# Performance work log

Hardware: AMD Instinct MI355X
Metric: run time of the kernel (lower is better)

The kernel has to match this reference:

```python
import jax, jax.numpy as jnp
import numpy as np
from jax import lax

CHANNEL = 64
HIDDEN = 128

def _conv(x, w, b):
    # x: [B, Cin, H, W], w: [Cout, Cin, 3, 3] -> [B, Cout, H, W], SAME padding
    y = lax.conv_general_dilated(x, w, window_strides=(1, 1), padding='SAME',
                                 dimension_numbers=('NCHW', 'OIHW', 'NCHW'))
    return y + b[None, :, None, None]

def setup_inputs() -> dict:
    key = jax.random.key(0)
    ks = jax.random.split(key, 5)
    T, B, C, H, W = 12, 2, CHANNEL, 128, 128
    x = jax.random.normal(ks[0], (T, B, C, H, W), dtype=jnp.float32)
    fan_g = (C + HIDDEN) * 9
    W_gates = jax.random.normal(ks[1], (4 * HIDDEN, C + HIDDEN, 3, 3), dtype=jnp.float32) / np.sqrt(fan_g)
    b_gates = jnp.zeros((4 * HIDDEN,), dtype=jnp.float32)
    W_out = jax.random.normal(ks[2], (C, HIDDEN, 3, 3), dtype=jnp.float32) / np.sqrt(HIDDEN * 9)
    b_out = jnp.zeros((C,), dtype=jnp.float32)
    return {'x': x, 'W_gates': W_gates, 'b_gates': b_gates, 'W_out': W_out, 'b_out': b_out}

def _convlstm_forward(x, W_gates, b_gates, W_out, b_out):
    T, B, C, H, W = x.shape
    h0 = jnp.zeros((B, HIDDEN, H, W), dtype=x.dtype)
    c0 = jnp.zeros((B, HIDDEN, H, W), dtype=x.dtype)

    def step(carry, xt):
        h, c = carry
        gates = _conv(jnp.concatenate([xt, h], axis=1), W_gates, b_gates)
        i_g, f_g, o_g, g_g = jnp.split(gates, 4, axis=1)
        c = jax.nn.sigmoid(f_g) * c + jax.nn.sigmoid(i_g) * jnp.tanh(g_g)
        h = jax.nn.sigmoid(o_g) * jnp.tanh(c)
        return (h, c), h

    _, hs = lax.scan(step, (h0, c0), x)          # hs: [T, B, HIDDEN, H, W]
    out = _conv(hs.reshape(T * B, HIDDEN, H, W), W_out, b_out)
    return out.reshape(T, B, C, H, W)

def reference(x, W_gates, b_gates, W_out, b_out):
    return _convlstm_forward(x, W_gates, b_gates, W_out, b_out)
```

## Files before the change

kernel.cpp:

```cpp
#include <hip/hip_runtime.h>

typedef _Float16 f16;
typedef __attribute__((ext_vector_type(8))) _Float16 f16x8;
typedef __attribute__((ext_vector_type(4))) float f32x4;
typedef __attribute__((ext_vector_type(16))) float f32x16;

#define SLICE_H 4326400


__device__ __forceinline__ void gld_lds16(void* lds, const void* g) {
  __builtin_amdgcn_global_load_lds(
      (const __attribute__((address_space(1))) void*)g,
      (__attribute__((address_space(3))) void*)lds, 16, 0, 0);
}

__device__ __forceinline__ float sigf(float v) { return 1.0f / (1.0f + __expf(-v)); }
__device__ __forceinline__ float tanh_fast(float v) { return 2.0f / (1.0f + __expf(-2.0f * v)) - 1.0f; }


__global__ __launch_bounds__(256) void kwt(const float* __restrict__ wsrc,
                                           f16* __restrict__ th, int R) {
  int idx = blockIdx.x * 256 + threadIdx.x;
  if (idx >= 9 * R) return;
  int tap = idx / R, r = idx - tap * R;
  th[idx] = (f16)wsrc[(size_t)r * 9 + tap];
}

__global__ __launch_bounds__(256) void kwtg(const float* __restrict__ wsrc,
                                            f16* __restrict__ th) {
  int idx = blockIdx.x * 256 + threadIdx.x;
  const int R = 512 * 192;
  if (idx >= 9 * R) return;
  int tap = idx / R, rr = idx - tap * R;
  int co = rr / 192, ci = rr - co * 192;
  int gate = co >> 7, hch = co & 127;
  int N = ((hch >> 6) << 8) + (((hch >> 5) & 1) << 7) + (gate << 5) + (hch & 31);
  th[(size_t)tap * R + (size_t)N * 192 + ci] = (f16)wsrc[(size_t)rr * 9 + tap];
}


__global__ __launch_bounds__(256) void kxform(const float* __restrict__ xt,
                                              f16* __restrict__ xp) {
  int pid = blockIdx.x * 256 + threadIdx.x;
  int b = pid >> 14, y = (pid >> 7) & 127, x = pid & 127;
  const float* src = xt + (size_t)b * 64 * 16384 + (size_t)y * 128 + x;
  size_t doff = ((size_t)((b * 130 + y + 1) * 130 + (x + 1))) * 64;
#pragma unroll
  for (int cc = 0; cc < 8; ++cc) {
    f16x8 vh;
#pragma unroll
    for (int j = 0; j < 8; ++j) vh[j] = (f16)src[(size_t)(cc * 8 + j) * 16384];
    *(f16x8*)(xp + doff + cc * 8) = vh;
  }
}


#define SMEM_G (25344 + 49152)

__global__ __launch_bounds__(256, 2) void kgates(
    const f16* __restrict__ xp, const f16* __restrict__ hp,
    const f16* __restrict__ wg, const float* __restrict__ bg,
    float* __restrict__ cbuf, f16* __restrict__ hslot) {
  extern __shared__ char smem[];
  f16* Ap = (f16*)smem;
  f16* Br = (f16*)(smem + 25344);
  const int tid = threadIdx.x;
  const int lane = tid & 63;
  const int w = tid >> 6;
  const int l31 = lane & 31;
  const int h5 = lane >> 5;
  const int wm = w >> 1, wn = w & 1;
  const int y = blockIdx.x;
  const int b = blockIdx.y;
  const int z = blockIdx.z;
  const int n0 = z * 256;
  const int chunk = (lane & 3) ^ ((lane >> 3) & 3);
  const int slotB0 = (h5 ^ ((l31 >> 1) & 3) ^ ((l31 >> 4) & 1)) << 3;

  f32x16 acc[2][4] = {};

  const f16* wgthr = wg + (size_t)(n0 + (lane >> 2)) * 192 +
                     (chunk ^ (w & 1)) * 8 + w * 3072;

  auto stageA = [&](int cig) {
    const f16* S; int CS, cigl;
    if (cig < 2) { S = xp; CS = 64;  cigl = cig; }
    else         { S = hp; CS = 128; cigl = cig - 2; }
    for (int i = w; i < 27; i += 4) {
      int dy = i / 9, sub = i - dy * 9;
      int xp0 = sub * 16;
      const f16* src = S +
          ((size_t)((b * 130 + y + dy) * 130 + xp0 + (lane >> 2))) * CS +
          cigl * 32 + (chunk ^ (sub & 1)) * 8;
      f16* dst = Ap + (dy * 132 + xp0) * 32;
      if (sub == 8) { if (lane < 16) gld_lds16(dst, src); }
      else gld_lds16(dst, src);
    }
  };
  auto stageB = [&](int j) {
    int cig = j / 9, tap = j - cig * 9;
    f16* dst = Br + (j % 3) * 8192 + w * 512;
    const f16* src = wgthr + (size_t)tap * (512 * 192) + cig * 32;
#pragma unroll
    for (int ii = 0; ii < 4; ++ii)
      gld_lds16(dst + ii * 2048, src + ii * 12288);
  };

  stageA(0);
  stageB(0);
  stageB(1);
  asm volatile("s_waitcnt vmcnt(4)" ::: "memory");
  __builtin_amdgcn_s_barrier();

  for (int j = 0; j < 54; ++j) {
    const int cig = j / 9, tap = j - cig * 9;
    const int dy = tap / 3, dx = tap - dy * 3;

    if (j + 2 < 54) stageB(j + 2);

    const f16* Bc = Br + (j % 3) * 8192;
    const int rr = l31 + dx;
    const int slotA0 = (h5 ^ ((rr >> 1) & 3) ^ ((rr >> 4) & 1)) << 3;
    const f16* arow = Ap + dy * (132 * 32) + (wm * 64 + rr) * 32;
    const f16* brow = Bc + (wn * 128 + l31) * 32;
    f16x8 af[2][2], bfr[4][2];
#pragma unroll
    for (int mt = 0; mt < 2; ++mt) {
      af[mt][0] = *(const f16x8*)(arow + mt * 1024 + slotA0);
      af[mt][1] = *(const f16x8*)(arow + mt * 1024 + (slotA0 ^ 16));
    }
#pragma unroll
    for (int nt = 0; nt < 4; ++nt) {
      bfr[nt][0] = *(const f16x8*)(brow + nt * 1024 + slotB0);
      bfr[nt][1] = *(const f16x8*)(brow + nt * 1024 + (slotB0 ^ 16));
    }

    __builtin_amdgcn_s_setprio(1);
#pragma unroll
    for (int k = 0; k < 2; ++k)
#pragma unroll
      for (int mt = 0; mt < 2; ++mt)
#pragma unroll
        for (int nt = 0; nt < 4; ++nt)
          acc[mt][nt] = __builtin_amdgcn_mfma_f32_32x32x16_f16(
              af[mt][k], bfr[nt][k], acc[mt][nt], 0, 0, 0);
    __builtin_amdgcn_s_setprio(0);

    if (tap == 8) {
      __builtin_amdgcn_s_barrier();
      if (cig < 5) stageA(cig + 1);
      asm volatile("s_waitcnt vmcnt(0)" ::: "memory");
      __builtin_amdgcn_s_barrier();
    } else {
      if (j + 2 < 54) asm volatile("s_waitcnt vmcnt(4)" ::: "memory");
      else            asm volatile("s_waitcnt vmcnt(0)" ::: "memory");
      __builtin_amdgcn_s_barrier();
    }
  }

  const int hch = z * 64 + wn * 32 + l31;
  const float bi  = bg[hch];
  const float bf2 = bg[128 + hch];
  const float bo2 = bg[256 + hch];
  const float bg2 = bg[384 + hch];
  float* crow = cbuf + ((size_t)(b * 128 + hch) * 128 + y) * 128;
  f16* hrow = hslot + ((size_t)((b * 130 + y + 1) * 130 + 1)) * 128 + hch;
#pragma unroll
  for (int mt = 0; mt < 2; ++mt) {
#pragma unroll
    for (int rq = 0; rq < 4; ++rq) {
      const int px0 = wm * 64 + mt * 32 + rq * 8 + h5 * 4;
      f32x4 co = *(const f32x4*)(crow + px0);
      f32x4 cn;
      f16 hv[4];
#pragma unroll
      for (int e = 0; e < 4; ++e) {
        const int reg = rq * 4 + e;
        float iv = sigf(acc[mt][0][reg] + bi);
        float fv = sigf(acc[mt][1][reg] + bf2);
        float ov = sigf(acc[mt][2][reg] + bo2);
        float gv = tanh_fast(acc[mt][3][reg] + bg2);
        float cv = fv * co[e] + iv * gv;
        cn[e] = cv;
        hv[e] = (f16)(ov * tanh_fast(cv));
      }
      *(f32x4*)(crow + px0) = cn;
#pragma unroll
      for (int e = 0; e < 4; ++e) hrow[(size_t)(px0 + e) * 128] = hv[e];
    }
  }
}


#define SMEM_O (25344 + 12288)

__global__ __launch_bounds__(256, 4) void koutconv(
    const f16* __restrict__ hr, int slot0, const f16* __restrict__ wo,
    const float* __restrict__ bo, float* __restrict__ outb) {
  extern __shared__ char smem[];
  f16* Ap = (f16*)smem;
  f16* Br = (f16*)(smem + 25344);
  const int tid = threadIdx.x, lane = tid & 63, w = tid >> 6;
  const int l31 = lane & 31, h5 = lane >> 5;
  const int y = blockIdx.x;
  const int b = blockIdx.y;
  const int ts = blockIdx.z;
  const f16* hp = hr + (size_t)((slot0 + ts) % 5) * SLICE_H;
  float* outt = outb + (size_t)ts * 2 * 64 * 16384;
  const int chunk = (lane & 3) ^ ((lane >> 3) & 3);
  const int slotB0 = (h5 ^ ((l31 >> 1) & 3) ^ ((l31 >> 4) & 1)) << 3;

  f32x16 acc[2] = {};

  const f16* wothr = wo + (size_t)(w * 16 + (lane >> 2)) * 128 +
                     (chunk ^ (w & 1)) * 8;

  auto stageA = [&](int cig) {
    for (int i = w; i < 27; i += 4) {
      int dy = i / 9, sub = i - dy * 9;
      int xp0 = sub * 16;
      const f16* src = hp +
          ((size_t)((b * 130 + y + dy) * 130 + xp0 + (lane >> 2))) * 128 +
          cig * 32 + (chunk ^ (sub & 1)) * 8;
      f16* dst = Ap + (dy * 132 + xp0) * 32;
      if (sub == 8) { if (lane < 16) gld_lds16(dst, src); }
      else gld_lds16(dst, src);
    }
  };
  auto stageB = [&](int j) {
    int cig = j / 9, tap = j - cig * 9;
    gld_lds16(Br + (j % 3) * 2048 + w * 512,
              wothr + (size_t)tap * (64 * 128) + cig * 32);
  };

  stageA(0);
  stageB(0);
  stageB(1);
  asm volatile("s_waitcnt vmcnt(1)" ::: "memory");
  __builtin_amdgcn_s_barrier();

  for (int cig = 0; cig < 4; ++cig) {
    for (int tap = 0; tap < 9; ++tap) {
      const int j = cig * 9 + tap;
      const int dy = tap / 3, dx = tap - dy * 3;

      if (j + 2 < 36) stageB(j + 2);

      const f16* Bc = Br + (j % 3) * 2048;
      const int rr = l31 + dx;
      const int slotA0 = (h5 ^ ((rr >> 1) & 3) ^ ((rr >> 4) & 1)) << 3;
      const f16* arow = Ap + dy * (132 * 32) + (w * 32 + rr) * 32;
      const f16* brow = Bc + l31 * 32;
      f16x8 af[2], bfr[2][2];
      af[0] = *(const f16x8*)(arow + slotA0);
      af[1] = *(const f16x8*)(arow + (slotA0 ^ 16));
#pragma unroll
      for (int nt = 0; nt < 2; ++nt) {
        bfr[nt][0] = *(const f16x8*)(brow + nt * 1024 + slotB0);
        bfr[nt][1] = *(const f16x8*)(brow + nt * 1024 + (slotB0 ^ 16));
      }

      __builtin_amdgcn_s_setprio(1);
#pragma unroll
      for (int k = 0; k < 2; ++k)
#pragma unroll
        for (int nt = 0; nt < 2; ++nt)
          acc[nt] = __builtin_amdgcn_mfma_f32_32x32x16_f16(
              af[k], bfr[nt][k], acc[nt], 0, 0, 0);
      __builtin_amdgcn_s_setprio(0);

      if (tap == 8) {
        __builtin_amdgcn_s_barrier();
        if (cig < 3) stageA(cig + 1);
        asm volatile("s_waitcnt vmcnt(0)" ::: "memory");
        __builtin_amdgcn_s_barrier();
      } else {
        if (j + 2 < 36) asm volatile("s_waitcnt vmcnt(1)" ::: "memory");
        else            asm volatile("s_waitcnt vmcnt(0)" ::: "memory");
        __builtin_amdgcn_s_barrier();
      }
    }
  }

#pragma unroll
  for (int nt = 0; nt < 2; ++nt) {
    const int cout = nt * 32 + l31;
    const float bias = bo[cout];
    float* orow = outt + (((size_t)b * 64 + cout) * 128 + y) * 128;
#pragma unroll
    for (int rq = 0; rq < 4; ++rq) {
      const int px0 = w * 32 + rq * 8 + h5 * 4;
      f32x4 v;
#pragma unroll
      for (int e = 0; e < 4; ++e) v[e] = acc[nt][rq * 4 + e] + bias;
      *(f32x4*)(orow + px0) = v;
    }
  }
}


extern "C" void kernel_launch(void* const* d_in, const int* in_sizes, int n_in,
                              void* d_out, int out_size, void* d_ws, size_t ws_size,
                              hipStream_t stream) {
  const float* x  = (const float*)d_in[0];
  const float* Wg = (const float*)d_in[1];
  const float* bg = (const float*)d_in[2];
  const float* Wo = (const float*)d_in[3];
  const float* bo = (const float*)d_in[4];
  float* out = (float*)d_out;

  char* base = (char*)d_ws;
  size_t off = 0;
  auto carve = [&](size_t bytes) {
    char* p = base + off;
    off += (bytes + 1023) & ~(size_t)1023;
    return p;
  };
  const size_t PADPOS = (size_t)2 * 130 * 130;
  const size_t xpad_b  = PADPOS * 64 * 2 + 1024;
  const size_t hring_b = (size_t)5 * SLICE_H * 2 + 1024;
  const size_t c_b = (size_t)2 * 128 * 128 * 128 * 4;

  f16* xp    = (f16*)carve(xpad_b);
  f16* hr    = (f16*)carve(hring_b);
  float* cbuf = (float*)carve(c_b);
  f16* wg    = (f16*)carve((size_t)9 * 512 * 192 * 2);
  f16* wo    = (f16*)carve((size_t)9 * 64 * 128 * 2);

  hipMemsetAsync(xp, 0, xpad_b, stream);
  hipMemsetAsync(hr, 0, hring_b, stream);
  hipMemsetAsync(cbuf, 0, c_b, stream);

  kwtg<<<(9 * 512 * 192 + 255) / 256, 256, 0, stream>>>(Wg, wg);
  kwt<<<(9 * 64 * 128 + 255) / 256, 256, 0, stream>>>(Wo, wo, 64 * 128);

  for (int t = 0; t < 12; ++t) {
    const float* xt = x + (size_t)t * 2 * 64 * 16384;
    kxform<<<128, 256, 0, stream>>>(xt, xp);
    kgates<<<dim3(128, 2, 2), 256, SMEM_G, stream>>>(
        xp, hr + (size_t)(t % 5) * SLICE_H, wg, bg, cbuf,
        hr + (size_t)((t + 1) % 5) * SLICE_H);
    if ((t & 3) == 3) {
      koutconv<<<dim3(128, 2, 4), 256, SMEM_O, stream>>>(
          hr, (t - 2) % 5, wo, bo, out + (size_t)(t - 3) * 2 * 64 * 16384);
    }
  }
}
```

Before: 1.084 ms.

## Load weight fragments directly from global into registers, dropping LDS staging

The weight tensors are re-laid out into MFMA-fragment order so each lane can load its B operands straight from global memory into registers, double-buffered one tap ahead. This removes the B-tile LDS ring buffer, its per-tap barriers and waitcnts, and frees LDS, which could allow more resident blocks. The risk is that global load latency is exposed per tap with only one tap of prefetch, and that register pressure rises from holding two fragment sets.

```diff
diff --git a/kernel.cpp b/kernel.cpp
--- a/kernel.cpp
+++ b/kernel.cpp
@@ -19,11 +19,15 @@
 
 
 __global__ __launch_bounds__(256) void kwt(const float* __restrict__ wsrc,
-                                           f16* __restrict__ th, int R) {
+                                           f16* __restrict__ th) {
   int idx = blockIdx.x * 256 + threadIdx.x;
+  const int R = 64 * 128;
   if (idx >= 9 * R) return;
   int tap = idx / R, r = idx - tap * R;
-  th[idx] = (f16)wsrc[(size_t)r * 9 + tap];
+  int co = r >> 7, ci = r & 127;
+  int cig = ci >> 5, k = (ci >> 4) & 1, pos = ci & 15;
+  th[((size_t)(cig * 9 + tap) * 2 + k) * 1024 + co * 16 + pos] =
+      (f16)wsrc[(size_t)r * 9 + tap];
 }
 
 __global__ __launch_bounds__(256) void kwtg(const float* __restrict__ wsrc,
@@ -35,7 +39,9 @@
   int co = rr / 192, ci = rr - co * 192;
   int gate = co >> 7, hch = co & 127;
   int N = ((hch >> 6) << 8) + (((hch >> 5) & 1) << 7) + (gate << 5) + (hch & 31);
-  th[(size_t)tap * R + (size_t)N * 192 + ci] = (f16)wsrc[(size_t)rr * 9 + tap];
+  int cig = ci >> 5, k = (ci >> 4) & 1, pos = ci & 15;
+  th[((size_t)(cig * 9 + tap) * 2 + k) * 8192 + N * 16 + pos] =
+      (f16)wsrc[(size_t)rr * 9 + tap];
 }
 
 
@@ -55,7 +61,7 @@
 }
 
 
-#define SMEM_G (25344 + 49152)
+#define SMEM_G 25344
 
 __global__ __launch_bounds__(256, 2) void kgates(
     const f16* __restrict__ xp, const f16* __restrict__ hp,
@@ -63,7 +69,6 @@
     float* __restrict__ cbuf, f16* __restrict__ hslot) {
   extern __shared__ char smem[];
   f16* Ap = (f16*)smem;
-  f16* Br = (f16*)(smem + 25344);
   const int tid = threadIdx.x;
   const int lane = tid & 63;
   const int w = tid >> 6;
@@ -75,12 +80,10 @@
   const int z = blockIdx.z;
   const int n0 = z * 256;
   const int chunk = (lane & 3) ^ ((lane >> 3) & 3);
-  const int slotB0 = (h5 ^ ((l31 >> 1) & 3) ^ ((l31 >> 4) & 1)) << 3;
 
   f32x16 acc[2][4] = {};
 
-  const f16* wgthr = wg + (size_t)(n0 + (lane >> 2)) * 192 +
-                     (chunk ^ (w & 1)) * 8 + w * 3072;
+  const f16* wgthr = wg + (size_t)(n0 + wn * 128 + l31) * 16 + h5 * 8;
 
   auto stageA = [&](int cig) {
     const f16* S; int CS, cigl;
@@ -97,44 +100,28 @@
       else gld_lds16(dst, src);
     }
   };
-  auto stageB = [&](int j) {
-    int cig = j / 9, tap = j - cig * 9;
-    f16* dst = Br + (j % 3) * 8192 + w * 512;
-    const f16* src = wgthr + (size_t)tap * (512 * 192) + cig * 32;
-#pragma unroll
-    for (int ii = 0; ii < 4; ++ii)
-      gld_lds16(dst + ii * 2048, src + ii * 12288);
-  };
-
-  stageA(0);
-  stageB(0);
-  stageB(1);
-  asm volatile("s_waitcnt vmcnt(4)" ::: "memory");
-  __builtin_amdgcn_s_barrier();
-
-  for (int j = 0; j < 54; ++j) {
+
+  struct BF { f16x8 v[8]; };
+  auto loadB = [&](int j2, BF& f) {
+    const f16* p = wgthr + (size_t)j2 * 16384;
+#pragma unroll
+    for (int nt = 0; nt < 4; ++nt)
+#pragma unroll
+      for (int k = 0; k < 2; ++k)
+        f.v[nt * 2 + k] = *(const f16x8*)(p + nt * 512 + k * 8192);
+  };
+  auto mfmaTap = [&](int j, const BF& bf) {
     const int cig = j / 9, tap = j - cig * 9;
     const int dy = tap / 3, dx = tap - dy * 3;
-
-    if (j + 2 < 54) stageB(j + 2);
-
-    const f16* Bc = Br + (j % 3) * 8192;
     const int rr = l31 + dx;
     const int slotA0 = (h5 ^ ((rr >> 1) & 3) ^ ((rr >> 4) & 1)) << 3;
     const f16* arow = Ap + dy * (132 * 32) + (wm * 64 + rr) * 32;
-    const f16* brow = Bc + (wn * 128 + l31) * 32;
-    f16x8 af[2][2], bfr[4][2];
+    f16x8 af[2][2];
 #pragma unroll
     for (int mt = 0; mt < 2; ++mt) {
       af[mt][0] = *(const f16x8*)(arow + mt * 1024 + slotA0);
       af[mt][1] = *(const f16x8*)(arow + mt * 1024 + (slotA0 ^ 16));
     }
-#pragma unroll
-    for (int nt = 0; nt < 4; ++nt) {
-      bfr[nt][0] = *(const f16x8*)(brow + nt * 1024 + slotB0);
-      bfr[nt][1] = *(const f16x8*)(brow + nt * 1024 + (slotB0 ^ 16));
-    }
-
     __builtin_amdgcn_s_setprio(1);
 #pragma unroll
     for (int k = 0; k < 2; ++k)
@@ -143,19 +130,29 @@
 #pragma unroll
         for (int nt = 0; nt < 4; ++nt)
           acc[mt][nt] = __builtin_amdgcn_mfma_f32_32x32x16_f16(
-              af[mt][k], bfr[nt][k], acc[mt][nt], 0, 0, 0);
+              af[mt][k], bf.v[nt * 2 + k], acc[mt][nt], 0, 0, 0);
     __builtin_amdgcn_s_setprio(0);
-
-    if (tap == 8) {
-      __builtin_amdgcn_s_barrier();
-      if (cig < 5) stageA(cig + 1);
-      asm volatile("s_waitcnt vmcnt(0)" ::: "memory");
-      __builtin_amdgcn_s_barrier();
-    } else {
-      if (j + 2 < 54) asm volatile("s_waitcnt vmcnt(4)" ::: "memory");
-      else            asm volatile("s_waitcnt vmcnt(0)" ::: "memory");
-      __builtin_amdgcn_s_barrier();
-    }
+  };
+  auto cigEnd = [&](int cig) {
+    __builtin_amdgcn_s_barrier();
+    if (cig < 5) stageA(cig + 1);
+    asm volatile("s_waitcnt vmcnt(0)" ::: "memory");
+    __builtin_amdgcn_s_barrier();
+  };
+
+  stageA(0);
+  BF b0, b1;
+  loadB(0, b0);
+  asm volatile("s_waitcnt vmcnt(0)" ::: "memory");
+  __builtin_amdgcn_s_barrier();
+
+  for (int j = 0; j < 54; j += 2) {
+    loadB(j + 1, b1);
+    mfmaTap(j, b0);
+    if (j % 9 == 8) cigEnd(j / 9);
+    if (j + 2 < 54) loadB(j + 2, b0);
+    mfmaTap(j + 1, b1);
+    if ((j + 1) % 9 == 8) cigEnd((j + 1) / 9);
   }
 
   const int hch = z * 64 + wn * 32 + l31;
@@ -192,14 +189,13 @@
 }
 
 
-#define SMEM_O (25344 + 12288)
+#define SMEM_O 25344
 
 __global__ __launch_bounds__(256, 4) void koutconv(
     const f16* __restrict__ hr, int slot0, const f16* __restrict__ wo,
     const float* __restrict__ bo, float* __restrict__ outb) {
   extern __shared__ char smem[];
   f16* Ap = (f16*)smem;
-  f16* Br = (f16*)(smem + 25344);
   const int tid = threadIdx.x, lane = tid & 63, w = tid >> 6;
   const int l31 = lane & 31, h5 = lane >> 5;
   const int y = blockIdx.x;
@@ -208,12 +204,10 @@
   const f16* hp = hr + (size_t)((slot0 + ts) % 5) * SLICE_H;
   float* outt = outb + (size_t)ts * 2 * 64 * 16384;
   const int chunk = (lane & 3) ^ ((lane >> 3) & 3);
-  const int slotB0 = (h5 ^ ((l31 >> 1) & 3) ^ ((l31 >> 4) & 1)) << 3;
 
   f32x16 acc[2] = {};
 
-  const f16* wothr = wo + (size_t)(w * 16 + (lane >> 2)) * 128 +
-                     (chunk ^ (w & 1)) * 8;
+  const f16* wothr = wo + (size_t)l31 * 16 + h5 * 8;
 
   auto stageA = [&](int cig) {
     for (int i = w; i < 27; i += 4) {
@@ -227,59 +221,54 @@
       else gld_lds16(dst, src);
     }
   };
-  auto stageB = [&](int j) {
-    int cig = j / 9, tap = j - cig * 9;
-    gld_lds16(Br + (j % 3) * 2048 + w * 512,
-              wothr + (size_t)tap * (64 * 128) + cig * 32);
+
+  struct BF { f16x8 v[4]; };
+  auto loadB = [&](int j2, BF& f) {
+    const f16* p = wothr + (size_t)j2 * 2048;
+#pragma unroll
+    for (int nt = 0; nt < 2; ++nt)
+#pragma unroll
+      for (int k = 0; k < 2; ++k)
+        f.v[nt * 2 + k] = *(const f16x8*)(p + nt * 512 + k * 1024);
+  };
+  auto mfmaTap = [&](int j, const BF& bf) {
+    const int cig = j / 9, tap = j - cig * 9;
+    const int dy = tap / 3, dx = tap - dy * 3;
+    const int rr = l31 + dx;
+    const int slotA0 = (h5 ^ ((rr >> 1) & 3) ^ ((rr >> 4) & 1)) << 3;
+    const f16* arow = Ap + dy * (132 * 32) + (w * 32 + rr) * 32;
+    f16x8 af[2];
+    af[0] = *(const f16x8*)(arow + slotA0);
+    af[1] = *(const f16x8*)(arow + (slotA0 ^ 16));
+    __builtin_amdgcn_s_setprio(1);
+#pragma unroll
+    for (int k = 0; k < 2; ++k)
+#pragma unroll
+      for (int nt = 0; nt < 2; ++nt)
+        acc[nt] = __builtin_amdgcn_mfma_f32_32x32x16_f16(
+            af[k], bf.v[nt * 2 + k], acc[nt], 0, 0, 0);
+    __builtin_amdgcn_s_setprio(0);
+  };
+  auto cigEnd = [&](int cig) {
+    __builtin_amdgcn_s_barrier();
+    if (cig < 3) stageA(cig + 1);
+    asm volatile("s_waitcnt vmcnt(0)" ::: "memory");
+    __builtin_amdgcn_s_barrier();
   };
 
   stageA(0);
-  stageB(0);
-  stageB(1);
-  asm volatile("s_waitcnt vmcnt(1)" ::: "memory");
+  BF b0, b1;
+  loadB(0, b0);
+  asm volatile("s_waitcnt vmcnt(0)" ::: "memory");
   __builtin_amdgcn_s_barrier();
 
-  for (int cig = 0; cig < 4; ++cig) {
-    for (int tap = 0; tap < 9; ++tap) {
-      const int j = cig * 9 + tap;
-      const int dy = tap / 3, dx = tap - dy * 3;
-
-      if (j + 2 < 36) stageB(j + 2);
-
-      const f16* Bc = Br + (j % 3) * 2048;
-      const int rr = l31 + dx;
-      const int slotA0 = (h5 ^ ((rr >> 1) & 3) ^ ((rr >> 4) & 1)) << 3;
-      const f16* arow = Ap + dy * (132 * 32) + (w * 32 + rr) * 32;
-      const f16* brow = Bc + l31 * 32;
-      f16x8 af[2], bfr[2][2];
-      af[0] = *(const f16x8*)(arow + slotA0);
-      af[1] = *(const f16x8*)(arow + (slotA0 ^ 16));
-#pragma unroll
-      for (int nt = 0; nt < 2; ++nt) {
-        bfr[nt][0] = *(const f16x8*)(brow + nt * 1024 + slotB0);
-        bfr[nt][1] = *(const f16x8*)(brow + nt * 1024 + (slotB0 ^ 16));
-      }
-
-      __builtin_amdgcn_s_setprio(1);
-#pragma unroll
-      for (int k = 0; k < 2; ++k)
-#pragma unroll
-        for (int nt = 0; nt < 2; ++nt)
-          acc[nt] = __builtin_amdgcn_mfma_f32_32x32x16_f16(
-              af[k], bfr[nt][k], acc[nt], 0, 0, 0);
-      __builtin_amdgcn_s_setprio(0);
-
-      if (tap == 8) {
-        __builtin_amdgcn_s_barrier();
-        if (cig < 3) stageA(cig + 1);
-        asm volatile("s_waitcnt vmcnt(0)" ::: "memory");
-        __builtin_amdgcn_s_barrier();
-      } else {
-        if (j + 2 < 36) asm volatile("s_waitcnt vmcnt(1)" ::: "memory");
-        else            asm volatile("s_waitcnt vmcnt(0)" ::: "memory");
-        __builtin_amdgcn_s_barrier();
-      }
-    }
+  for (int j = 0; j < 36; j += 2) {
+    loadB(j + 1, b1);
+    mfmaTap(j, b0);
+    if (j % 9 == 8) cigEnd(j / 9);
+    if (j + 2 < 36) loadB(j + 2, b0);
+    mfmaTap(j + 1, b1);
+    if ((j + 1) % 9 == 8) cigEnd((j + 1) / 9);
   }
 
 #pragma unroll
@@ -324,15 +313,15 @@
   f16* xp    = (f16*)carve(xpad_b);
   f16* hr    = (f16*)carve(hring_b);
   float* cbuf = (float*)carve(c_b);
-  f16* wg    = (f16*)carve((size_t)9 * 512 * 192 * 2);
-  f16* wo    = (f16*)carve((size_t)9 * 64 * 128 * 2);
+  f16* wg    = (f16*)carve((size_t)54 * 2 * 512 * 16 * 2);
+  f16* wo    = (f16*)carve((size_t)36 * 2 * 64 * 16 * 2);
 
   hipMemsetAsync(xp, 0, xpad_b, stream);
   hipMemsetAsync(hr, 0, hring_b, stream);
   hipMemsetAsync(cbuf, 0, c_b, stream);
 
   kwtg<<<(9 * 512 * 192 + 255) / 256, 256, 0, stream>>>(Wg, wg);
-  kwt<<<(9 * 64 * 128 + 255) / 256, 256, 0, stream>>>(Wo, wo, 64 * 128);
+  kwt<<<(9 * 64 * 128 + 255) / 256, 256, 0, stream>>>(Wo, wo);
 
   for (int t = 0; t < 12; ++t) {
     const float* xt = x + (size_t)t * 2 * 64 * 16384;
```

Result: no change. 1.080 ms (-0.3%).
